# Kernel tuning notes

Measured on AMD Instinct MI355X. Metric: run time of the kernel, lower is better.

Reference implementation:

```python
import jax, jax.numpy as jnp
import numpy as np

IN, H, FC1, FC2, OUT = 3, 30, 64, 32, 1
B, T = 8192, 256


def _lstm_layer(xT, W_ih, W_hh, b_ih, b_hh):
    """xT: (T, B, Din). Returns (hidden sequence (T,B,H), final h (B,H)).
    PyTorch gate order: i, f, g, o."""
    # Precompute input contribution for all timesteps (one big GEMM).
    gx = jnp.einsum('tbd,gd->tbg', xT, W_ih) + b_ih + b_hh  # (T,B,4H)
    b = xT.shape[1]
    h0 = jnp.zeros((b, W_hh.shape[1]), xT.dtype)
    c0 = h0

    def step(carry, g):
        h, c = carry
        gates = g + h @ W_hh.T
        i, f, gg, o = jnp.split(gates, 4, axis=-1)
        i = jax.nn.sigmoid(i)
        f = jax.nn.sigmoid(f)
        gg = jnp.tanh(gg)
        o = jax.nn.sigmoid(o)
        c = f * c + i * gg
        h = o * jnp.tanh(c)
        return (h, c), h

    (h_n, _), ys = jax.lax.scan(step, (h0, c0), gx)
    return ys, h_n


def setup_inputs() -> dict:
    key = jax.random.key(0)
    ks = jax.random.split(key, 16)
    s = 0.18  # ~1/sqrt(hidden_size), matches PyTorch uniform init scale
    inp = {
        'x': jax.random.normal(ks[0], (B, T, IN), jnp.float32),
        'W_ih0': jax.random.normal(ks[1], (4 * H, IN), jnp.float32) * s,
        'W_hh0': jax.random.normal(ks[2], (4 * H, H), jnp.float32) * s,
        'b_ih0': jax.random.normal(ks[3], (4 * H,), jnp.float32) * s,
        'b_hh0': jax.random.normal(ks[4], (4 * H,), jnp.float32) * s,
        'W_ih1': jax.random.normal(ks[5], (4 * H, H), jnp.float32) * s,
        'W_hh1': jax.random.normal(ks[6], (4 * H, H), jnp.float32) * s,
        'b_ih1': jax.random.normal(ks[7], (4 * H,), jnp.float32) * s,
        'b_hh1': jax.random.normal(ks[8], (4 * H,), jnp.float32) * s,
        'W_fc1': jax.random.normal(ks[9], (FC1, H), jnp.float32) * s,
        'b_fc1': jax.random.normal(ks[10], (FC1,), jnp.float32) * s,
        'W_fc2': jax.random.normal(ks[11], (FC2, FC1), jnp.float32) * 0.125,
        'b_fc2': jax.random.normal(ks[12], (FC2,), jnp.float32) * 0.125,
        'W_fc3': jax.random.normal(ks[13], (OUT, FC2), jnp.float32) * 0.17,
        'b_fc3': jax.random.normal(ks[14], (OUT,), jnp.float32) * 0.17,
    }
    return inp


def reference(x, W_ih0, W_hh0, b_ih0, b_hh0, W_ih1, W_hh1, b_ih1, b_hh1,
              W_fc1, b_fc1, W_fc2, b_fc2, W_fc3, b_fc3):
    xT = jnp.swapaxes(x, 0, 1)  # (T,B,IN)
    ys, _ = _lstm_layer(xT, W_ih0, W_hh0, b_ih0, b_hh0)   # layer 0 sequence
    _, h_n = _lstm_layer(ys, W_ih1, W_hh1, b_ih1, b_hh1)  # layer 1 final h
    # FC head (dropout = identity in eval mode)
    z = jax.nn.relu(h_n @ W_fc1.T + b_fc1)
    z = jax.nn.relu(z @ W_fc2.T + b_fc2)
    z = jax.nn.sigmoid(z @ W_fc3.T + b_fc3)
    return z.squeeze(-1)  # (B,)
```

## Files before the change

kernel.cpp:

```cpp
#include <hip/hip_runtime.h>

#define TT    256
#define HID   30
#define LOG2E 1.4426950408889634f
#define HS    40
#define NR    16
#define CHUNK 8

typedef __bf16 bf16x8_t __attribute__((ext_vector_type(8)));
typedef float  f32x4_t  __attribute__((ext_vector_type(4)));
typedef unsigned int u32x4_t __attribute__((ext_vector_type(4)));

__device__ __forceinline__ float fexp2(float x){
#if __has_builtin(__builtin_amdgcn_exp2f)
    return __builtin_amdgcn_exp2f(x);
#else
    return exp2f(x);
#endif
}
__device__ __forceinline__ float frcp(float x){
#if __has_builtin(__builtin_amdgcn_rcpf)
    return __builtin_amdgcn_rcpf(x);
#else
    return 1.f/x;
#endif
}
__device__ __forceinline__ float fsigmoid(float x){ return frcp(1.f + fexp2(-LOG2E*x)); }
__device__ __forceinline__ f32x4_t exp4(f32x4_t v){
    f32x4_t e; e[0]=fexp2(v[0]); e[1]=fexp2(v[1]); e[2]=fexp2(v[2]); e[3]=fexp2(v[3]); return e;
}
__device__ __forceinline__ f32x4_t rcp4(f32x4_t v){
    f32x4_t r; r[0]=frcp(v[0]); r[1]=frcp(v[1]); r[2]=frcp(v[2]); r[3]=frcp(v[3]); return r;
}

__device__ __forceinline__ uint32_t pk_bf16(float lo, float hi){
    uint32_t r;
    asm("v_cvt_pk_bf16_f32 %0, %1, %2" : "=v"(r) : "v"(lo), "v"(hi));
    return r;
}

__device__ __forceinline__ f32x4_t lstm_act(f32x4_t aI, f32x4_t aF, f32x4_t aG,
                                            f32x4_t aO, f32x4_t& cst){
    f32x4_t eI = exp4(aI);
    f32x4_t eF = exp4(aF);
    f32x4_t eG = exp4(aG);
    f32x4_t eO = exp4(aO);
    f32x4_t D1 = eF + 1.f;
    f32x4_t tG = eG + 1.f;
    f32x4_t D2 = eI*tG + tG;
    f32x4_t r  = rcp4(D1*D2);
    f32x4_t f  = r*D2;
    f32x4_t p  = (eG - 1.f) * (r*D1);
    cst = f*cst + p;
    f32x4_t cc;
    cc[0]=fminf(fmaxf(cst[0],-30.f),30.f);
    cc[1]=fminf(fmaxf(cst[1],-30.f),30.f);
    cc[2]=fminf(fmaxf(cst[2],-30.f),30.f);
    cc[3]=fminf(fmaxf(cst[3],-30.f),30.f);
    f32x4_t eC = exp4(cc * (2.f*LOG2E));
    f32x4_t tC = eC + 1.f;
    f32x4_t dn = eO*tC + tC;
    return (eC - 1.f) * rcp4(dn);
}

__global__ __launch_bounds__(128, 1)
void lstm_fused(const float* __restrict__ x,
    const float* __restrict__ Wih0, const float* __restrict__ Whh0,
    const float* __restrict__ bih0, const float* __restrict__ bhh0,
    const float* __restrict__ Wih1, const float* __restrict__ Whh1,
    const float* __restrict__ bih1, const float* __restrict__ bhh1,
    const float* __restrict__ Wfc1, const float* __restrict__ bfc1,
    const float* __restrict__ Wfc2, const float* __restrict__ bfc2,
    const float* __restrict__ Wfc3, const float* __restrict__ bfc3,
    float* __restrict__ out)
{
    __shared__ __align__(16) __bf16 ring[NR][16][HS];
    __shared__ __align__(4)  __bf16 xlds01[TT+1][16][2];
    __shared__ __align__(16) float  xlds2[TT][16];
    __shared__ float h1_last[16][32];
    __shared__ float zbuf[16][64];
    __shared__ float z2buf[16][32];

    const int tid  = threadIdx.x;
    const int lane = tid & 63;
    const int wv   = tid >> 6;
    const int n    = lane & 15;
    const int q    = lane >> 4;
    const int q4   = q*4;
    const int bbase = blockIdx.x * 16;

    {
        const float* xg = x + (size_t)bbase*(TT*3);
        for (int i4 = tid*4; i4 < 16*TT*3; i4 += 128*4) {
            int row = i4 / (TT*3), tc0 = i4 % (TT*3);
            f32x4_t v = *(const f32x4_t*)(xg + (size_t)row*(TT*3) + tc0);
            #pragma unroll
            for (int j = 0; j < 4; ++j) {
                int tc = tc0 + j;
                int t = tc/3, c = tc - 3*t;
                if (c == 2) xlds2[t][row] = v[j];
                else        xlds01[t][row][c] = (__bf16)v[j];
            }
        }
        if (tid < 32) xlds01[TT][tid>>1][tid&1] = (__bf16)0.f;
    }

    const int  ad01 = 4*(n + 32*(q & 1));
    const int  ad23 = ad01 + 64;
    const bool qlo  = (q < 2);
    const bool q3   = (q == 3);

    __syncthreads();

#define MF(A,B,C) __builtin_amdgcn_mfma_f32_16x16x32_bf16((A),(B),(C),0,0,0)
#define BP(a,s)   ((uint32_t)__builtin_amdgcn_ds_bpermute((a),(int)(s)))
#define XPOSE(hA, hB, XW, dst) do {                                            \
    uint32_t a01=pk_bf16((hA)[0],(hA)[1]), a23=pk_bf16((hA)[2],(hA)[3]);       \
    uint32_t b01=pk_bf16((hB)[0],(hB)[1]), b23=pk_bf16((hB)[2],(hB)[3]);       \
    uint32_t t0a=BP(ad01,a01), t1a=BP(ad01,a23), t2a=BP(ad23,a01), t3a=BP(ad23,a23); \
    uint32_t t0b=BP(ad01,b01), t1b=BP(ad01,b23), t2b=BP(ad23,b01), t3b=BP(ad23,b23); \
    u32x4_t fw;                                                                \
    fw[0] = qlo ? t0a : t0b;                                                   \
    fw[1] = qlo ? t1a : t1b;                                                   \
    fw[2] = qlo ? t2a : t2b;                                                   \
    fw[3] = q3 ? (XW) : (qlo ? t3a : t3b);                                     \
    (dst) = __builtin_bit_cast(bf16x8_t, fw);                                  \
} while (0)

    const float scl[4] = {-LOG2E, -LOG2E, 2.f*LOG2E, -LOG2E};

    if (wv == 0) {
        bf16x8_t w0[4][2];
        f32x4_t  bq0[4][2], wxq[4][2];
        #pragma unroll
        for (int g = 0; g < 4; ++g) {
            #pragma unroll
            for (int ch = 0; ch < 2; ++ch) {
                const float sg = scl[g];
                const int uf = ch*16 + n;
                const int uqf = (uf < HID) ? uf : 0;
                const int rowf = g*HID + uqf;
                bf16x8_t a{};
                #pragma unroll
                for (int j = 0; j < 8; ++j) {
                    const int k = q*8 + j;
                    float va;
                    if (k < HID)       va = Whh0[rowf*HID + k];
                    else if (k == 30)  va = Wih0[rowf*3 + 0];
                    else               va = Wih0[rowf*3 + 1];
                    a[j] = (__bf16)(sg*va);
                }
                w0[g][ch] = a;
                f32x4_t b0v, wxv;
                #pragma unroll
                for (int r = 0; r < 4; ++r) {
                    const int ub = ch*16 + q4 + r;
                    const int uqb = (ub < HID) ? ub : 0;
                    const int rowb = g*HID + uqb;
                    b0v[r] = sg*(bih0[rowb] + bhh0[rowb]);
                    wxv[r] = sg*Wih0[rowb*3 + 2];
                }
                bq0[g][ch] = b0v;  wxq[g][ch] = wxv;
            }
        }

        bf16x8_t h0frag;
        {
            u32x4_t z = {0u,0u,0u,0u};
            if (q3) z[3] = *(const uint32_t*)&xlds01[0][n][0];
            h0frag = __builtin_bit_cast(bf16x8_t, z);
        }
        f32x4_t c0A = {0,0,0,0}, c0B = {0,0,0,0};

        #pragma unroll 1
        for (int c = 0; c <= TT/CHUNK; ++c) {
            if (c < TT/CHUNK) {
                const int sb   = c*CHUNK;
                const int half = (c & 1)*CHUNK;
                #pragma unroll
                for (int j = 0; j < CHUNK; ++j) {
                    const int s = sb + j;
                    const float x2v = xlds2[s][n];
                    f32x4_t aI0 = MF(w0[0][0], h0frag, bq0[0][0] + wxq[0][0]*x2v);
                    f32x4_t aF0 = MF(w0[1][0], h0frag, bq0[1][0] + wxq[1][0]*x2v);
                    f32x4_t aG0 = MF(w0[2][0], h0frag, bq0[2][0] + wxq[2][0]*x2v);
                    f32x4_t aO0 = MF(w0[3][0], h0frag, bq0[3][0] + wxq[3][0]*x2v);
                    f32x4_t aI1 = MF(w0[0][1], h0frag, bq0[0][1] + wxq[0][1]*x2v);
                    f32x4_t aF1 = MF(w0[1][1], h0frag, bq0[1][1] + wxq[1][1]*x2v);
                    f32x4_t aG1 = MF(w0[2][1], h0frag, bq0[2][1] + wxq[2][1]*x2v);
                    f32x4_t aO1 = MF(w0[3][1], h0frag, bq0[3][1] + wxq[3][1]*x2v);
                    f32x4_t h0A = lstm_act(aI0, aF0, aG0, aO0, c0A);
                    f32x4_t h0B = lstm_act(aI1, aF1, aG1, aO1, c0B);
                    const uint32_t XW = *(const uint32_t*)&xlds01[s+1][n][0];
                    XPOSE(h0A, h0B, XW, h0frag);
                    *(bf16x8_t*)&ring[half + j][n][q*8] = h0frag;
                }
            }
            __syncthreads();
        }
    } else {
        bf16x8_t wi1[4][2], wh1[4][2];
        f32x4_t  bq1[4][2];
        #pragma unroll
        for (int g = 0; g < 4; ++g) {
            #pragma unroll
            for (int ch = 0; ch < 2; ++ch) {
                const float sg = scl[g];
                const int uf = ch*16 + n;
                const int uqf = (uf < HID) ? uf : 0;
                const int rowf = g*HID + uqf;
                bf16x8_t a{}, b{};
                #pragma unroll
                for (int j = 0; j < 8; ++j) {
                    const int k = q*8 + j;
                    float va = 0.f, vb = 0.f;
                    if (k < HID) { va = Wih1[rowf*HID + k];  vb = Whh1[rowf*HID + k]; }
                    a[j] = (__bf16)(sg*va);
                    b[j] = (__bf16)(sg*vb);
                }
                wi1[g][ch] = a;  wh1[g][ch] = b;
                f32x4_t b1v;
                #pragma unroll
                for (int r = 0; r < 4; ++r) {
                    const int ub = ch*16 + q4 + r;
                    const int uqb = (ub < HID) ? ub : 0;
                    const int rowb = g*HID + uqb;
                    b1v[r] = sg*(bih1[rowb] + bhh1[rowb]);
                }
                bq1[g][ch] = b1v;
            }
        }

        bf16x8_t h1frag;
        { u32x4_t z = {0u,0u,0u,0u}; h1frag = __builtin_bit_cast(bf16x8_t, z); }
        f32x4_t c1A = {0,0,0,0}, c1B = {0,0,0,0};

        #pragma unroll 1
        for (int c = 0; c <= TT/CHUNK; ++c) {
            if (c > 0) {
                const int cc   = c - 1;
                const int sb   = cc*CHUNK;
                const int half = (cc & 1)*CHUNK;
                #pragma unroll
                for (int j = 0; j < CHUNK; ++j) {
                    const int s = sb + j;
                    bf16x8_t A1 = *(const bf16x8_t*)&ring[half + j][n][q*8];
                    f32x4_t dI0 = MF(wi1[0][0], A1, bq1[0][0]);
                    f32x4_t dF0 = MF(wi1[1][0], A1, bq1[1][0]);
                    f32x4_t dG0 = MF(wi1[2][0], A1, bq1[2][0]);
                    f32x4_t dO0 = MF(wi1[3][0], A1, bq1[3][0]);
                    f32x4_t dI1 = MF(wi1[0][1], A1, bq1[0][1]);
                    f32x4_t dF1 = MF(wi1[1][1], A1, bq1[1][1]);
                    f32x4_t dG1 = MF(wi1[2][1], A1, bq1[2][1]);
                    f32x4_t dO1 = MF(wi1[3][1], A1, bq1[3][1]);
                    dI0 = MF(wh1[0][0], h1frag, dI0);
                    dF0 = MF(wh1[1][0], h1frag, dF0);
                    dG0 = MF(wh1[2][0], h1frag, dG0);
                    dO0 = MF(wh1[3][0], h1frag, dO0);
                    dI1 = MF(wh1[0][1], h1frag, dI1);
                    dF1 = MF(wh1[1][1], h1frag, dF1);
                    dG1 = MF(wh1[2][1], h1frag, dG1);
                    dO1 = MF(wh1[3][1], h1frag, dO1);
                    f32x4_t h1A = lstm_act(dI0, dF0, dG0, dO0, c1A);
                    f32x4_t h1B = lstm_act(dI1, dF1, dG1, dO1, c1B);
                    if (s == TT-1) {
                        *(f32x4_t*)&h1_last[n][q4]    = h1A;
                        *(f32x4_t*)&h1_last[n][16+q4] = h1B;
                    } else {
                        XPOSE(h1A, h1B, 0u, h1frag);
                    }
                }
            }
            __syncthreads();
        }
    }
#undef XPOSE
#undef BP
#undef MF

    #pragma unroll
    for (int rep = 0; rep < 8; ++rep) {
        int idx = tid + rep*128;
        int m = idx >> 6, uu = idx & 63;
        float a = bfc1[uu];
        for (int k = 0; k < HID; ++k) a += h1_last[m][k] * Wfc1[uu*HID+k];
        zbuf[m][uu] = fmaxf(a, 0.f);
    }
    __syncthreads();
    #pragma unroll
    for (int rep = 0; rep < 4; ++rep) {
        int idx = tid + rep*128;
        int m = idx >> 5, v = idx & 31;
        float a = bfc2[v];
        for (int k = 0; k < 64; ++k) a += zbuf[m][k] * Wfc2[v*64+k];
        z2buf[m][v] = fmaxf(a, 0.f);
    }
    __syncthreads();
    if (tid < 16) {
        float a = bfc3[0];
        for (int k = 0; k < 32; ++k) a += z2buf[tid][k] * Wfc3[k];
        out[bbase + tid] = fsigmoid(a);
    }
}

extern "C" void kernel_launch(void* const* d_in, const int* in_sizes, int n_in,
                              void* d_out, int out_size, void* d_ws, size_t ws_size,
                              hipStream_t stream) {
    const float* x    = (const float*)d_in[0];
    const float* Wih0 = (const float*)d_in[1];
    const float* Whh0 = (const float*)d_in[2];
    const float* bih0 = (const float*)d_in[3];
    const float* bhh0 = (const float*)d_in[4];
    const float* Wih1 = (const float*)d_in[5];
    const float* Whh1 = (const float*)d_in[6];
    const float* bih1 = (const float*)d_in[7];
    const float* bhh1 = (const float*)d_in[8];
    const float* Wfc1 = (const float*)d_in[9];
    const float* bfc1 = (const float*)d_in[10];
    const float* Wfc2 = (const float*)d_in[11];
    const float* bfc2 = (const float*)d_in[12];
    const float* Wfc3 = (const float*)d_in[13];
    const float* bfc3 = (const float*)d_in[14];
    float* outp = (float*)d_out;

    hipLaunchKernelGGL(lstm_fused, dim3(512), dim3(128), 0, stream,
        x, Wih0, Whh0, bih0, bhh0, Wih1, Whh1, bih1, bhh1,
        Wfc1, bfc1, Wfc2, bfc2, Wfc3, bfc3, outp);
}
```

Before: 285.6 us.

## Pack two 16-row LSTM pipelines per block and stream x from global into registers

Each block now runs two independent layer0/layer1 wave pairs covering 32 batch rows, so the grid halves to 256 blocks of 256 threads. The x staging through shared memory (and its initial barrier) is removed. Each layer-0 lane instead prefetches the next chunk of inputs from global memory into registers while computing the current chunk. This aims to cut LDS footprint and prologue latency and to hide input load latency. The trade-off is that the two pipes now share block-wide barriers and the kernel uses more registers.

```diff
diff --git a/kernel.cpp b/kernel.cpp
--- a/kernel.cpp
+++ b/kernel.cpp
@@ -63,7 +63,7 @@
     return (eC - 1.f) * rcp4(dn);
 }
 
-__global__ __launch_bounds__(128, 1)
+__global__ __launch_bounds__(256, 1)
 void lstm_fused(const float* __restrict__ x,
     const float* __restrict__ Wih0, const float* __restrict__ Whh0,
     const float* __restrict__ bih0, const float* __restrict__ bhh0,
@@ -74,43 +74,26 @@
     const float* __restrict__ Wfc3, const float* __restrict__ bfc3,
     float* __restrict__ out)
 {
-    __shared__ __align__(16) __bf16 ring[NR][16][HS];
-    __shared__ __align__(4)  __bf16 xlds01[TT+1][16][2];
-    __shared__ __align__(16) float  xlds2[TT][16];
-    __shared__ float h1_last[16][32];
-    __shared__ float zbuf[16][64];
-    __shared__ float z2buf[16][32];
+    __shared__ __align__(16) __bf16 ring[2][NR][16][HS];
+    __shared__ float h1_last[32][32];
+    __shared__ float zbuf[32][64];
+    __shared__ float z2buf[32][32];
 
     const int tid  = threadIdx.x;
     const int lane = tid & 63;
     const int wv   = tid >> 6;
+    const int pipe = wv >> 1;
+    const int role = wv & 1;
     const int n    = lane & 15;
     const int q    = lane >> 4;
     const int q4   = q*4;
-    const int bbase = blockIdx.x * 16;
-
-    {
-        const float* xg = x + (size_t)bbase*(TT*3);
-        for (int i4 = tid*4; i4 < 16*TT*3; i4 += 128*4) {
-            int row = i4 / (TT*3), tc0 = i4 % (TT*3);
-            f32x4_t v = *(const f32x4_t*)(xg + (size_t)row*(TT*3) + tc0);
-            #pragma unroll
-            for (int j = 0; j < 4; ++j) {
-                int tc = tc0 + j;
-                int t = tc/3, c = tc - 3*t;
-                if (c == 2) xlds2[t][row] = v[j];
-                else        xlds01[t][row][c] = (__bf16)v[j];
-            }
-        }
-        if (tid < 32) xlds01[TT][tid>>1][tid&1] = (__bf16)0.f;
-    }
+    const int brow  = blockIdx.x * 32;
+    const int bbase = brow + pipe*16;
 
     const int  ad01 = 4*(n + 32*(q & 1));
     const int  ad23 = ad01 + 64;
     const bool qlo  = (q < 2);
     const bool q3   = (q == 3);
-
-    __syncthreads();
 
 #define MF(A,B,C) __builtin_amdgcn_mfma_f32_16x16x32_bf16((A),(B),(C),0,0,0)
 #define BP(a,s)   ((uint32_t)__builtin_amdgcn_ds_bpermute((a),(int)(s)))
@@ -129,7 +112,7 @@
 
     const float scl[4] = {-LOG2E, -LOG2E, 2.f*LOG2E, -LOG2E};
 
-    if (wv == 0) {
+    if (role == 0) {
         bf16x8_t w0[4][2];
         f32x4_t  bq0[4][2], wxq[4][2];
         #pragma unroll
@@ -164,10 +147,18 @@
             }
         }
 
+        const float* xr = x + (size_t)(bbase + n) * (TT*3);
+        float cx0[CHUNK], cx1[CHUNK], cx2[CHUNK];
+        float nx0[CHUNK], nx1[CHUNK], nx2[CHUNK];
+        #pragma unroll
+        for (int j = 0; j < CHUNK; ++j) {
+            cx0[j]=xr[3*j]; cx1[j]=xr[3*j+1]; cx2[j]=xr[3*j+2];
+        }
+
         bf16x8_t h0frag;
         {
             u32x4_t z = {0u,0u,0u,0u};
-            if (q3) z[3] = *(const uint32_t*)&xlds01[0][n][0];
+            if (q3) z[3] = pk_bf16(cx0[0], cx1[0]);
             h0frag = __builtin_bit_cast(bf16x8_t, z);
         }
         f32x4_t c0A = {0,0,0,0}, c0B = {0,0,0,0};
@@ -175,12 +166,18 @@
         #pragma unroll 1
         for (int c = 0; c <= TT/CHUNK; ++c) {
             if (c < TT/CHUNK) {
-                const int sb   = c*CHUNK;
+                {
+                    const int nb = (c+1)*CHUNK;
+                    #pragma unroll
+                    for (int j = 0; j < CHUNK; ++j) {
+                        int tp = nb + j;  if (tp > TT-1) tp = TT-1;
+                        nx0[j]=xr[3*tp]; nx1[j]=xr[3*tp+1]; nx2[j]=xr[3*tp+2];
+                    }
+                }
                 const int half = (c & 1)*CHUNK;
                 #pragma unroll
                 for (int j = 0; j < CHUNK; ++j) {
-                    const int s = sb + j;
-                    const float x2v = xlds2[s][n];
+                    const float x2v = cx2[j];
                     f32x4_t aI0 = MF(w0[0][0], h0frag, bq0[0][0] + wxq[0][0]*x2v);
                     f32x4_t aF0 = MF(w0[1][0], h0frag, bq0[1][0] + wxq[1][0]*x2v);
                     f32x4_t aG0 = MF(w0[2][0], h0frag, bq0[2][0] + wxq[2][0]*x2v);
@@ -191,9 +188,14 @@
                     f32x4_t aO1 = MF(w0[3][1], h0frag, bq0[3][1] + wxq[3][1]*x2v);
                     f32x4_t h0A = lstm_act(aI0, aF0, aG0, aO0, c0A);
                     f32x4_t h0B = lstm_act(aI1, aF1, aG1, aO1, c0B);
-                    const uint32_t XW = *(const uint32_t*)&xlds01[s+1][n][0];
+                    const uint32_t XW = (j < CHUNK-1) ? pk_bf16(cx0[j+1], cx1[j+1])
+                                                      : pk_bf16(nx0[0],  nx1[0]);
                     XPOSE(h0A, h0B, XW, h0frag);
-                    *(bf16x8_t*)&ring[half + j][n][q*8] = h0frag;
+                    *(bf16x8_t*)&ring[pipe][half + j][n][q*8] = h0frag;
+                }
+                #pragma unroll
+                for (int j = 0; j < CHUNK; ++j) {
+                    cx0[j]=nx0[j]; cx1[j]=nx1[j]; cx2[j]=nx2[j];
                 }
             }
             __syncthreads();
@@ -244,7 +246,7 @@
                 #pragma unroll
                 for (int j = 0; j < CHUNK; ++j) {
                     const int s = sb + j;
-                    bf16x8_t A1 = *(const bf16x8_t*)&ring[half + j][n][q*8];
+                    bf16x8_t A1 = *(const bf16x8_t*)&ring[pipe][half + j][n][q*8];
                     f32x4_t dI0 = MF(wi1[0][0], A1, bq1[0][0]);
                     f32x4_t dF0 = MF(wi1[1][0], A1, bq1[1][0]);
                     f32x4_t dG0 = MF(wi1[2][0], A1, bq1[2][0]);
@@ -264,8 +266,8 @@
                     f32x4_t h1A = lstm_act(dI0, dF0, dG0, dO0, c1A);
                     f32x4_t h1B = lstm_act(dI1, dF1, dG1, dO1, c1B);
                     if (s == TT-1) {
-                        *(f32x4_t*)&h1_last[n][q4]    = h1A;
-                        *(f32x4_t*)&h1_last[n][16+q4] = h1B;
+                        *(f32x4_t*)&h1_last[pipe*16 + n][q4]    = h1A;
+                        *(f32x4_t*)&h1_last[pipe*16 + n][16+q4] = h1B;
                     } else {
                         XPOSE(h1A, h1B, 0u, h1frag);
                     }
@@ -280,7 +282,7 @@
 
     #pragma unroll
     for (int rep = 0; rep < 8; ++rep) {
-        int idx = tid + rep*128;
+        int idx = tid + rep*256;
         int m = idx >> 6, uu = idx & 63;
         float a = bfc1[uu];
         for (int k = 0; k < HID; ++k) a += h1_last[m][k] * Wfc1[uu*HID+k];
@@ -289,17 +291,17 @@
     __syncthreads();
     #pragma unroll
     for (int rep = 0; rep < 4; ++rep) {
-        int idx = tid + rep*128;
+        int idx = tid + rep*256;
         int m = idx >> 5, v = idx & 31;
         float a = bfc2[v];
         for (int k = 0; k < 64; ++k) a += zbuf[m][k] * Wfc2[v*64+k];
         z2buf[m][v] = fmaxf(a, 0.f);
     }
     __syncthreads();
-    if (tid < 16) {
+    if (tid < 32) {
         float a = bfc3[0];
         for (int k = 0; k < 32; ++k) a += z2buf[tid][k] * Wfc3[k];
-        out[bbase + tid] = fsigmoid(a);
+        out[brow + tid] = fsigmoid(a);
     }
 }
 
@@ -323,7 +325,7 @@
     const float* bfc3 = (const float*)d_in[14];
     float* outp = (float*)d_out;
 
-    hipLaunchKernelGGL(lstm_fused, dim3(512), dim3(128), 0, stream,
+    hipLaunchKernelGGL(lstm_fused, dim3(256), dim3(256), 0, stream,
         x, Wih0, Whh0, bih0, bhh0, Wih1, Whh1, bih1, bhh1,
         Wfc1, bfc1, Wfc2, bfc2, Wfc3, bfc3, outp);
 }
```

Result: faster. 277.9 us (-2.7%).
